# Kernel optimization log

Hardware: AMD Instinct MI355X
Metric: run time of the kernel (lower is better)

## Reference

```python
import jax, jax.numpy as jnp
import numpy as np

N_NODES = 50000
N_EDGES = 1600000
N_GRAPHS = 512
VOCAB = 1000
EMB = 32
HID = 64
N_CLASS = 2


def setup_inputs() -> dict:
    key = jax.random.key(0)
    ks = jax.random.split(key, 12)
    x_ids = jax.random.randint(ks[0], (N_NODES,), 0, VOCAB)
    edge_index = jax.random.randint(ks[1], (2, N_EDGES), 0, N_NODES)
    batch = jnp.sort(jax.random.randint(ks[2], (N_NODES,), 0, N_GRAPHS))
    def s(k, shape, fan):
        return jax.random.normal(k, shape, jnp.float32) * (1.0 / np.sqrt(fan))
    return {
        "x_ids": x_ids,
        "edge_index": edge_index,
        "batch": batch,
        "embed": s(ks[3], (VOCAB, EMB), EMB),
        "w1_l": s(ks[4], (EMB, HID), EMB),
        "b1": jnp.zeros((HID,), jnp.float32),
        "w1_r": s(ks[5], (EMB, HID), EMB),
        "w2_l": s(ks[6], (HID, HID), HID),
        "b2": jnp.zeros((HID,), jnp.float32),
        "w2_r": s(ks[7], (HID, HID), HID),
        "w_out": s(ks[8], (HID, N_CLASS), HID),
        "b_out": jnp.zeros((N_CLASS,), jnp.float32),
    }


def _sage(x, src, dst, w_l, b, w_r):
    # PyG SAGEConv (aggr='mean'): out = lin_l(mean_{j in N(i)} x_j) + lin_r(x_i)
    msg_sum = jax.ops.segment_sum(x[src], dst, num_segments=N_NODES)  # [N, d]
    deg = jax.ops.segment_sum(jnp.ones((src.shape[0],), x.dtype), dst,
                              num_segments=N_NODES)
    mean = msg_sum / jnp.maximum(deg, 1.0)[:, None]
    return mean @ w_l + b + x @ w_r


def reference(x_ids, edge_index, batch, embed, w1_l, b1, w1_r,
              w2_l, b2, w2_r, w_out, b_out):
    src, dst = edge_index[0], edge_index[1]
    x = embed[x_ids]                                  # [N, emb]
    x = jax.nn.relu(_sage(x, src, dst, w1_l, b1, w1_r))  # [N, hid]
    x = jax.nn.relu(_sage(x, src, dst, w2_l, b2, w2_r))  # [N, hid]
    # global_mean_pool over batch segments
    gsum = jax.ops.segment_sum(x, batch, num_segments=N_GRAPHS)
    gcnt = jax.ops.segment_sum(jnp.ones((N_NODES,), x.dtype), batch,
                               num_segments=N_GRAPHS)
    pooled = gsum / jnp.maximum(gcnt, 1.0)[:, None]   # [G, hid]
    return pooled @ w_out + b_out                     # [G, n_class]
```

## Files before the change

kernel.cpp:

```cpp
#include <hip/hip_runtime.h>
#include <hip/hip_bf16.h>

#define N_NODES 50000
#define N_EDGES 1600000
#define N_GRAPHS 512
#define VOCAB 1000
#define EMB 32
#define HID 64
#define N_CLASS 2

#define MAXDEG 96

#define NVEC (N_EDGES / 4)
#define SORT_VPB 1024
#define SORT_BLOCKS ((NVEC + SORT_VPB - 1) / SORT_VPB)
#define BSHIFT 8
#define BUCKET_NODES 256
#define NBUCK ((N_NODES + BUCKET_NODES - 1) / BUCKET_NODES)

#define L2P_BLOCKS 768
#define L2P_WAVES (L2P_BLOCKS * 4)
#define L2P_CHUNK ((N_NODES + L2P_WAVES - 1) / L2P_WAVES)

typedef int iv4 __attribute__((ext_vector_type(4)));
typedef unsigned long long u64;

__device__ __forceinline__ float rdlane(float v, int k) {
    return __int_as_float(__builtin_amdgcn_readlane(__float_as_int(v), k));
}

__global__ __launch_bounds__(256) void hist_kernel(const int* __restrict__ dst,
                                                   int* __restrict__ hist) {
    __shared__ int lh[NBUCK];
    for (int b = threadIdx.x; b < NBUCK; b += 256) lh[b] = 0;
    __syncthreads();
    const iv4* dst4 = (const iv4*)dst;
    int vbase = blockIdx.x * SORT_VPB;
    #pragma unroll
    for (int t = 0; t < 4; ++t) {
        int v = vbase + t * 256 + threadIdx.x;
        if (v < NVEC) {
            iv4 d4 = __builtin_nontemporal_load(&dst4[v]);
            atomicAdd(&lh[d4.x >> BSHIFT], 1);
            atomicAdd(&lh[d4.y >> BSHIFT], 1);
            atomicAdd(&lh[d4.z >> BSHIFT], 1);
            atomicAdd(&lh[d4.w >> BSHIFT], 1);
        }
    }
    __syncthreads();
    for (int b = threadIdx.x; b < NBUCK; b += 256)
        hist[b * SORT_BLOCKS + blockIdx.x] = lh[b];
}

__global__ __launch_bounds__(256) void scan_rows_kernel(int* __restrict__ hist,
                                                        int* __restrict__ btot) {
    int* row = hist + (size_t)blockIdx.x * SORT_BLOCKS;
    __shared__ int wsum[4];
    int tid = threadIdx.x, lane = tid & 63, w = tid >> 6;
    int carry = 0;
    for (int base = 0; base < SORT_BLOCKS; base += 256) {
        int idx = base + tid;
        int v = (idx < SORT_BLOCKS) ? row[idx] : 0;
        int inc = v;
        #pragma unroll
        for (int off = 1; off < 64; off <<= 1) {
            int n = __shfl_up(inc, off, 64);
            if (lane >= off) inc += n;
        }
        if (lane == 63) wsum[w] = inc;
        __syncthreads();
        int woff = 0;
        #pragma unroll
        for (int k = 0; k < 4; ++k) if (k < w) woff += wsum[k];
        if (idx < SORT_BLOCKS) row[idx] = carry + woff + inc - v;
        carry += wsum[0] + wsum[1] + wsum[2] + wsum[3];
        __syncthreads();
    }
    if (tid == 0) btot[blockIdx.x] = carry;
}

__global__ __launch_bounds__(256) void scan_btot_kernel(const int* __restrict__ btot,
                                                        int* __restrict__ boff) {
    __shared__ int wsum[4];
    int tid = threadIdx.x, lane = tid & 63, w = tid >> 6;
    int v = (tid < NBUCK) ? btot[tid] : 0;
    int inc = v;
    #pragma unroll
    for (int off = 1; off < 64; off <<= 1) {
        int n = __shfl_up(inc, off, 64);
        if (lane >= off) inc += n;
    }
    if (lane == 63) wsum[w] = inc;
    __syncthreads();
    int woff = 0;
    #pragma unroll
    for (int k = 0; k < 4; ++k) if (k < w) woff += wsum[k];
    if (tid < NBUCK) boff[tid] = woff + inc - v;
    if (tid == 0) boff[NBUCK] = wsum[0] + wsum[1] + wsum[2] + wsum[3];
}

__global__ __launch_bounds__(256) void scatter_kernel(const int* __restrict__ src,
        const int* __restrict__ dst, const int* __restrict__ x_ids,
        const int* __restrict__ hist, const int* __restrict__ boff,
        u64* __restrict__ ebuf) {
    __shared__ int lbase[NBUCK];
    for (int b = threadIdx.x; b < NBUCK; b += 256)
        lbase[b] = hist[b * SORT_BLOCKS + blockIdx.x] + boff[b];
    __syncthreads();
    const iv4* dst4 = (const iv4*)dst;
    const iv4* src4 = (const iv4*)src;
    int vbase = blockIdx.x * SORT_VPB;
    #pragma unroll
    for (int t = 0; t < 4; ++t) {
        int v = vbase + t * 256 + threadIdx.x;
        if (v < NVEC) {
            iv4 d4 = __builtin_nontemporal_load(&dst4[v]);
            iv4 s4 = __builtin_nontemporal_load(&src4[v]);
            int pay0 = (x_ids[s4.x] << 16) | s4.x;
            int pay1 = (x_ids[s4.y] << 16) | s4.y;
            int pay2 = (x_ids[s4.z] << 16) | s4.z;
            int pay3 = (x_ids[s4.w] << 16) | s4.w;
            int p0 = atomicAdd(&lbase[d4.x >> BSHIFT], 1);
            int p1 = atomicAdd(&lbase[d4.y >> BSHIFT], 1);
            int p2 = atomicAdd(&lbase[d4.z >> BSHIFT], 1);
            int p3 = atomicAdd(&lbase[d4.w >> BSHIFT], 1);
            ebuf[p0] = ((u64)(unsigned)d4.x << 32) | (unsigned)pay0;
            ebuf[p1] = ((u64)(unsigned)d4.y << 32) | (unsigned)pay1;
            ebuf[p2] = ((u64)(unsigned)d4.z << 32) | (unsigned)pay2;
            ebuf[p3] = ((u64)(unsigned)d4.w << 32) | (unsigned)pay3;
        }
    }
}

__global__ __launch_bounds__(256) void csr_bucket_kernel(const u64* __restrict__ ebuf,
        const int* __restrict__ boff, int* __restrict__ cursor, int* __restrict__ csr) {
    int b = blockIdx.x;
    __shared__ int cur[BUCKET_NODES];
    for (int r = threadIdx.x; r < BUCKET_NODES; r += 256) cur[r] = 0;
    __syncthreads();
    int base = boff[b];
    int end  = boff[b + 1];
    int node0 = b << BSHIFT;
    for (int i = base + threadIdx.x; i < end; i += 256) {
        u64 e = ebuf[i];
        int d = (int)(e >> 32);
        int pay = (int)(e & 0xffffffffu);
        int pos = atomicAdd(&cur[d - node0], 1);
        csr[d * MAXDEG + pos] = pay;
    }
    __syncthreads();
    for (int r = threadIdx.x; r < BUCKET_NODES; r += 256) {
        int d = node0 + r;
        if (d < N_NODES) cursor[d] = cur[r];
    }
}

__global__ void precompute_e1_kernel(const float* __restrict__ embed,
                                     const float* __restrict__ w1l,
                                     const float* __restrict__ w1r,
                                     __hip_bfloat16* __restrict__ e1b,
                                     float* __restrict__ e1r) {
    int id = blockIdx.x * blockDim.x + threadIdx.x;
    if (id >= VOCAB * HID) return;
    int v = id >> 6, j = id & 63;
    float a = 0.0f, b = 0.0f;
    #pragma unroll
    for (int k = 0; k < EMB; ++k) {
        float ev = embed[v * EMB + k];
        a = fmaf(ev, w1l[k * HID + j], a);
        b = fmaf(ev, w1r[k * HID + j], b);
    }
    e1b[id] = __float2bfloat16(a);
    e1r[id] = b;
}

__global__ __launch_bounds__(256) void agg1_lin1_kernel(
        const int* __restrict__ x_ids, const int* __restrict__ csr,
        const int* __restrict__ deg_arr, const __hip_bfloat16* __restrict__ e1b,
        const float* __restrict__ e1r, const float* __restrict__ b1,
        float* __restrict__ h1, __hip_bfloat16* __restrict__ h1b) {
    int id = blockIdx.x * blockDim.x + threadIdx.x;
    int i = __builtin_amdgcn_readfirstlane(id >> 6);
    int j = threadIdx.x & 63;
    int s = i * MAXDEG;
    int deg = deg_arr[i];
    int e = s + deg;
    float s0 = 0.f, s1 = 0.f, s2 = 0.f, s3 = 0.f;
    float s4 = 0.f, s5 = 0.f, s6 = 0.f, s7 = 0.f;
    int k = s;
    for (; k + 8 <= e; k += 8) {
        int c0 = csr[k]     >> 16, c1 = csr[k + 1] >> 16;
        int c2 = csr[k + 2] >> 16, c3 = csr[k + 3] >> 16;
        int c4 = csr[k + 4] >> 16, c5 = csr[k + 5] >> 16;
        int c6 = csr[k + 6] >> 16, c7 = csr[k + 7] >> 16;
        s0 += (float)e1b[c0 * HID + j];
        s1 += (float)e1b[c1 * HID + j];
        s2 += (float)e1b[c2 * HID + j];
        s3 += (float)e1b[c3 * HID + j];
        s4 += (float)e1b[c4 * HID + j];
        s5 += (float)e1b[c5 * HID + j];
        s6 += (float)e1b[c6 * HID + j];
        s7 += (float)e1b[c7 * HID + j];
    }
    for (; k < e; ++k) s0 += (float)e1b[(csr[k] >> 16) * HID + j];
    float mean = ((s0 + s1) + (s2 + s3) + (s4 + s5) + (s6 + s7)) / fmaxf((float)deg, 1.0f);
    float h = fmaxf(mean + b1[j] + e1r[x_ids[i] * HID + j], 0.0f);
    int o = i * HID + j;
    h1[o] = h;
    h1b[o] = __float2bfloat16(h);
}

__global__ __launch_bounds__(256) void agg2_mean_kernel(
        const __hip_bfloat16* __restrict__ h1b, const int* __restrict__ csr,
        const int* __restrict__ deg_arr, float* __restrict__ mean2) {
    int id = blockIdx.x * blockDim.x + threadIdx.x;
    int i = __builtin_amdgcn_readfirstlane(id >> 6);
    int j = threadIdx.x & 63;
    int s = i * MAXDEG;
    int deg = deg_arr[i];
    int e = s + deg;
    float s0 = 0.f, s1 = 0.f, s2 = 0.f, s3 = 0.f;
    float s4 = 0.f, s5 = 0.f, s6 = 0.f, s7 = 0.f;
    int k = s;
    for (; k + 8 <= e; k += 8) {
        int n0 = csr[k]     & 0xFFFF, n1 = csr[k + 1] & 0xFFFF;
        int n2 = csr[k + 2] & 0xFFFF, n3 = csr[k + 3] & 0xFFFF;
        int n4 = csr[k + 4] & 0xFFFF, n5 = csr[k + 5] & 0xFFFF;
        int n6 = csr[k + 6] & 0xFFFF, n7 = csr[k + 7] & 0xFFFF;
        s0 += (float)h1b[n0 * HID + j];
        s1 += (float)h1b[n1 * HID + j];
        s2 += (float)h1b[n2 * HID + j];
        s3 += (float)h1b[n3 * HID + j];
        s4 += (float)h1b[n4 * HID + j];
        s5 += (float)h1b[n5 * HID + j];
        s6 += (float)h1b[n6 * HID + j];
        s7 += (float)h1b[n7 * HID + j];
    }
    for (; k < e; ++k) s0 += (float)h1b[(csr[k] & 0xFFFF) * HID + j];
    float mean = ((s0 + s1) + (s2 + s3) + (s4 + s5) + (s6 + s7)) / fmaxf((float)deg, 1.0f);
    mean2[i * HID + j] = mean;
}

__global__ __launch_bounds__(256) void lin2_pool_kernel(
        const float* __restrict__ mean2, const float* __restrict__ h1,
        const float* __restrict__ w2l, const float* __restrict__ b2,
        const float* __restrict__ w2r, const int* __restrict__ batch,
        float* __restrict__ gsum) {
    int lane = threadIdx.x & 63;
    int wv = (blockIdx.x * blockDim.x + threadIdx.x) >> 6;
    int i0 = wv * L2P_CHUNK;
    int i1 = i0 + L2P_CHUNK; if (i1 > N_NODES) i1 = N_NODES;
    if (i0 >= N_NODES) return;
    float wl[HID], wr[HID];
    #pragma unroll
    for (int k = 0; k < HID; ++k) {
        wl[k] = w2l[k * HID + lane];
        wr[k] = w2r[k * HID + lane];
    }
    float bj = b2[lane];
    int curg = __builtin_amdgcn_readfirstlane(batch[i0]);
    float accp = 0.0f;
    float m = mean2[i0 * HID + lane];
    float h = h1[i0 * HID + lane];
    for (int i = i0; i < i1; ++i) {
        float mn = 0.f, hn = 0.f;
        if (i + 1 < i1) {
            mn = mean2[(i + 1) * HID + lane];
            hn = h1[(i + 1) * HID + lane];
        }
        int g = __builtin_amdgcn_readfirstlane(batch[i]);
        if (g != curg) {
            atomicAdd(&gsum[curg * HID + lane], accp);
            accp = 0.0f;
            curg = g;
        }
        float z = bj;
        #pragma unroll
        for (int k = 0; k < HID; ++k)
            z = fmaf(rdlane(m, k), wl[k], fmaf(rdlane(h, k), wr[k], z));
        accp += fmaxf(z, 0.0f);
        m = mn; h = hn;
    }
    atomicAdd(&gsum[curg * HID + lane], accp);
}

__global__ void out_kernel(const float* __restrict__ gsum, const int* __restrict__ batch,
                           const float* __restrict__ w_out, const float* __restrict__ b_out,
                           float* __restrict__ out) {
    int id = blockIdx.x * blockDim.x + threadIdx.x;
    if (id >= N_GRAPHS * N_CLASS) return;
    int g = id >> 1, c = id & 1;
    int lo = 0, hi = N_NODES;
    while (lo < hi) { int mid = (lo + hi) >> 1; if (batch[mid] < g) lo = mid + 1; else hi = mid; }
    int first = lo;
    lo = 0; hi = N_NODES;
    while (lo < hi) { int mid = (lo + hi) >> 1; if (batch[mid] <= g) lo = mid + 1; else hi = mid; }
    float cnt = (float)(lo - first);
    float inv = 1.0f / fmaxf(cnt, 1.0f);
    float acc = b_out[c];
    #pragma unroll
    for (int j = 0; j < HID; ++j)
        acc = fmaf(gsum[g * HID + j] * inv, w_out[j * N_CLASS + c], acc);
    out[id] = acc;
}


extern "C" void kernel_launch(void* const* d_in, const int* in_sizes, int n_in,
                              void* d_out, int out_size, void* d_ws, size_t ws_size,
                              hipStream_t stream) {
    const int*   x_ids = (const int*)d_in[0];
    const int*   edge  = (const int*)d_in[1];
    const int*   batch = (const int*)d_in[2];
    const float* embed = (const float*)d_in[3];
    const float* w1l   = (const float*)d_in[4];
    const float* b1    = (const float*)d_in[5];
    const float* w1r   = (const float*)d_in[6];
    const float* w2l   = (const float*)d_in[7];
    const float* b2    = (const float*)d_in[8];
    const float* w2r   = (const float*)d_in[9];
    const float* wout  = (const float*)d_in[10];
    const float* bout  = (const float*)d_in[11];
    const int* src = edge;
    const int* dst = edge + N_EDGES;
    float* out = (float*)d_out;

    char* ws = (char*)d_ws;
    size_t off = 0;
    auto alloc = [&](size_t bytes) -> void* {
        void* p = ws + off;
        off += (bytes + 255) & ~(size_t)255;
        return p;
    };
    float*           h1     = (float*)alloc((size_t)N_NODES * HID * 4);
    __hip_bfloat16*  h1b    = (__hip_bfloat16*)alloc((size_t)N_NODES * HID * 2);
    float*           mean2  = (float*)alloc((size_t)N_NODES * HID * 4);
    int*             csr    = (int*)alloc((size_t)N_NODES * MAXDEG * 4);
    int*             cursor = (int*)alloc((size_t)N_NODES * 4);
    int*             hist   = (int*)alloc((size_t)NBUCK * SORT_BLOCKS * 4);
    int*             btot   = (int*)alloc((size_t)NBUCK * 4);
    int*             boff   = (int*)alloc((size_t)(NBUCK + 1) * 4);
    __hip_bfloat16*  e1b    = (__hip_bfloat16*)alloc((size_t)VOCAB * HID * 2);
    float*           e1r    = (float*)alloc((size_t)VOCAB * HID * 4);
    float*           gsum   = (float*)alloc((size_t)N_GRAPHS * HID * 4);

    u64* ebuf = (u64*)mean2;

    hipMemsetAsync(gsum, 0, (size_t)N_GRAPHS * HID * 4, stream);

    const int B = 256;
    precompute_e1_kernel<<<(VOCAB * HID + B - 1) / B, B, 0, stream>>>(embed, w1l, w1r, e1b, e1r);

    hist_kernel<<<SORT_BLOCKS, B, 0, stream>>>(dst, hist);
    scan_rows_kernel<<<NBUCK, B, 0, stream>>>(hist, btot);
    scan_btot_kernel<<<1, B, 0, stream>>>(btot, boff);
    scatter_kernel<<<SORT_BLOCKS, B, 0, stream>>>(src, dst, x_ids, hist, boff, ebuf);
    csr_bucket_kernel<<<NBUCK, B, 0, stream>>>(ebuf, boff, cursor, csr);

    agg1_lin1_kernel<<<N_NODES * HID / B, B, 0, stream>>>(x_ids, csr, cursor,
                                                          e1b, e1r, b1, h1, h1b);
    agg2_mean_kernel<<<N_NODES * HID / B, B, 0, stream>>>(h1b, csr, cursor, mean2);
    lin2_pool_kernel<<<L2P_BLOCKS, B, 0, stream>>>(mean2, h1, w2l, b2, w2r, batch, gsum);
    out_kernel<<<(N_GRAPHS * N_CLASS + B - 1) / B, B, 0, stream>>>(gsum, batch, wout, bout, out);
}
```

Measured before the change: 232.5 us.

## Process eight nodes per wave with 16-byte vectorized bf16 row gathers in aggregation

Both neighbor-aggregation kernels are remapped so that each wave handles 8 nodes instead of one. Each lane owns 8 contiguous features and loads them with a single 16-byte load, replacing one 2-byte load per lane per neighbor. CSR indices are read four at a time, and outputs are written as vector stores. This is meant to cut the memory instruction count and the per-neighbor scalar overhead of the gathers. In exchange, lanes within a wave now follow different node degrees, which adds divergence, and the iv4 CSR read can go past the node's degree into padding slots.

```diff
diff --git a/kernel.cpp b/kernel.cpp
--- a/kernel.cpp
+++ b/kernel.cpp
@@ -18,13 +18,29 @@
 #define BUCKET_NODES 256
 #define NBUCK ((N_NODES + BUCKET_NODES - 1) / BUCKET_NODES)
 
+#define AGG_THREADS (N_NODES * 8)
+#define AGG_BLOCKS ((AGG_THREADS + 255) / 256)
+
 #define L2P_BLOCKS 768
 #define L2P_WAVES (L2P_BLOCKS * 4)
 #define L2P_CHUNK ((N_NODES + L2P_WAVES - 1) / L2P_WAVES)
 
 typedef int iv4 __attribute__((ext_vector_type(4)));
+typedef unsigned short us;
+typedef us usv8 __attribute__((ext_vector_type(8)));
+typedef float fv4 __attribute__((ext_vector_type(4)));
 typedef unsigned long long u64;
 
+__device__ __forceinline__ float bf2f(us u) {
+    union { unsigned int i; float f; } c;
+    c.i = ((unsigned int)u) << 16;
+    return c.f;
+}
+__device__ __forceinline__ us f2bf(float f) {
+    union { __hip_bfloat16 b; us u; } c;
+    c.b = __float2bfloat16(f);
+    return c.u;
+}
 __device__ __forceinline__ float rdlane(float v, int k) {
     return __int_as_float(__builtin_amdgcn_readlane(__float_as_int(v), k));
 }
@@ -158,7 +174,7 @@
 __global__ void precompute_e1_kernel(const float* __restrict__ embed,
                                      const float* __restrict__ w1l,
                                      const float* __restrict__ w1r,
-                                     __hip_bfloat16* __restrict__ e1b,
+                                     us* __restrict__ e1b,
                                      float* __restrict__ e1r) {
     int id = blockIdx.x * blockDim.x + threadIdx.x;
     if (id >= VOCAB * HID) return;
@@ -170,75 +186,93 @@
         a = fmaf(ev, w1l[k * HID + j], a);
         b = fmaf(ev, w1r[k * HID + j], b);
     }
-    e1b[id] = __float2bfloat16(a);
+    e1b[id] = f2bf(a);
     e1r[id] = b;
 }
 
 __global__ __launch_bounds__(256) void agg1_lin1_kernel(
         const int* __restrict__ x_ids, const int* __restrict__ csr,
-        const int* __restrict__ deg_arr, const __hip_bfloat16* __restrict__ e1b,
+        const int* __restrict__ deg_arr, const us* __restrict__ e1b,
         const float* __restrict__ e1r, const float* __restrict__ b1,
-        float* __restrict__ h1, __hip_bfloat16* __restrict__ h1b) {
-    int id = blockIdx.x * blockDim.x + threadIdx.x;
-    int i = __builtin_amdgcn_readfirstlane(id >> 6);
-    int j = threadIdx.x & 63;
-    int s = i * MAXDEG;
-    int deg = deg_arr[i];
-    int e = s + deg;
-    float s0 = 0.f, s1 = 0.f, s2 = 0.f, s3 = 0.f;
-    float s4 = 0.f, s5 = 0.f, s6 = 0.f, s7 = 0.f;
-    int k = s;
-    for (; k + 8 <= e; k += 8) {
-        int c0 = csr[k]     >> 16, c1 = csr[k + 1] >> 16;
-        int c2 = csr[k + 2] >> 16, c3 = csr[k + 3] >> 16;
-        int c4 = csr[k + 4] >> 16, c5 = csr[k + 5] >> 16;
-        int c6 = csr[k + 6] >> 16, c7 = csr[k + 7] >> 16;
-        s0 += (float)e1b[c0 * HID + j];
-        s1 += (float)e1b[c1 * HID + j];
-        s2 += (float)e1b[c2 * HID + j];
-        s3 += (float)e1b[c3 * HID + j];
-        s4 += (float)e1b[c4 * HID + j];
-        s5 += (float)e1b[c5 * HID + j];
-        s6 += (float)e1b[c6 * HID + j];
-        s7 += (float)e1b[c7 * HID + j];
-    }
-    for (; k < e; ++k) s0 += (float)e1b[(csr[k] >> 16) * HID + j];
-    float mean = ((s0 + s1) + (s2 + s3) + (s4 + s5) + (s6 + s7)) / fmaxf((float)deg, 1.0f);
-    float h = fmaxf(mean + b1[j] + e1r[x_ids[i] * HID + j], 0.0f);
-    int o = i * HID + j;
-    h1[o] = h;
-    h1b[o] = __float2bfloat16(h);
+        float* __restrict__ h1, us* __restrict__ h1b) {
+    int tid = blockIdx.x * blockDim.x + threadIdx.x;
+    int lane = threadIdx.x & 63;
+    int g = lane >> 3, c8 = lane & 7;
+    int node = (tid >> 6) * 8 + g;
+    bool valid = node < N_NODES;
+    int nclamp = valid ? node : 0;
+    int deg = valid ? deg_arr[nclamp] : 0;
+    const int* crow = csr + (size_t)nclamp * MAXDEG;
+    float a0=0.f,a1=0.f,a2=0.f,a3=0.f,a4=0.f,a5=0.f,a6=0.f,a7=0.f;
+    for (int k = 0; k < deg; k += 4) {
+        iv4 cv = *(const iv4*)(crow + k);
+        #define GATH1(CVAL, T)                                                   \
+        if (k + (T) < deg) {                                                     \
+            int cls = (CVAL) >> 16;                                              \
+            usv8 r = *(const usv8*)(e1b + cls * HID + c8 * 8);                   \
+            a0 += bf2f(r[0]); a1 += bf2f(r[1]); a2 += bf2f(r[2]); a3 += bf2f(r[3]); \
+            a4 += bf2f(r[4]); a5 += bf2f(r[5]); a6 += bf2f(r[6]); a7 += bf2f(r[7]); \
+        }
+        GATH1(cv.x, 0) GATH1(cv.y, 1) GATH1(cv.z, 2) GATH1(cv.w, 3)
+        #undef GATH1
+    }
+    if (!valid) return;
+    float inv = 1.0f / fmaxf((float)deg, 1.0f);
+    int xid = x_ids[nclamp];
+    const fv4* er = (const fv4*)(e1r + xid * HID + c8 * 8);
+    fv4 e0 = er[0], e1v = er[1];
+    const fv4* bb = (const fv4*)(b1 + c8 * 8);
+    fv4 b0 = bb[0], b1v = bb[1];
+    fv4 h0, h1v;
+    h0.x = fmaxf(a0 * inv + b0.x + e0.x, 0.0f);
+    h0.y = fmaxf(a1 * inv + b0.y + e0.y, 0.0f);
+    h0.z = fmaxf(a2 * inv + b0.z + e0.z, 0.0f);
+    h0.w = fmaxf(a3 * inv + b0.w + e0.w, 0.0f);
+    h1v.x = fmaxf(a4 * inv + b1v.x + e1v.x, 0.0f);
+    h1v.y = fmaxf(a5 * inv + b1v.y + e1v.y, 0.0f);
+    h1v.z = fmaxf(a6 * inv + b1v.z + e1v.z, 0.0f);
+    h1v.w = fmaxf(a7 * inv + b1v.w + e1v.w, 0.0f);
+    int o = node * HID + c8 * 8;
+    *(fv4*)(h1 + o) = h0;
+    *(fv4*)(h1 + o + 4) = h1v;
+    usv8 hb;
+    hb[0] = f2bf(h0.x); hb[1] = f2bf(h0.y); hb[2] = f2bf(h0.z); hb[3] = f2bf(h0.w);
+    hb[4] = f2bf(h1v.x); hb[5] = f2bf(h1v.y); hb[6] = f2bf(h1v.z); hb[7] = f2bf(h1v.w);
+    *(usv8*)(h1b + o) = hb;
 }
 
 __global__ __launch_bounds__(256) void agg2_mean_kernel(
-        const __hip_bfloat16* __restrict__ h1b, const int* __restrict__ csr,
+        const us* __restrict__ h1b, const int* __restrict__ csr,
         const int* __restrict__ deg_arr, float* __restrict__ mean2) {
-    int id = blockIdx.x * blockDim.x + threadIdx.x;
-    int i = __builtin_amdgcn_readfirstlane(id >> 6);
-    int j = threadIdx.x & 63;
-    int s = i * MAXDEG;
-    int deg = deg_arr[i];
-    int e = s + deg;
-    float s0 = 0.f, s1 = 0.f, s2 = 0.f, s3 = 0.f;
-    float s4 = 0.f, s5 = 0.f, s6 = 0.f, s7 = 0.f;
-    int k = s;
-    for (; k + 8 <= e; k += 8) {
-        int n0 = csr[k]     & 0xFFFF, n1 = csr[k + 1] & 0xFFFF;
-        int n2 = csr[k + 2] & 0xFFFF, n3 = csr[k + 3] & 0xFFFF;
-        int n4 = csr[k + 4] & 0xFFFF, n5 = csr[k + 5] & 0xFFFF;
-        int n6 = csr[k + 6] & 0xFFFF, n7 = csr[k + 7] & 0xFFFF;
-        s0 += (float)h1b[n0 * HID + j];
-        s1 += (float)h1b[n1 * HID + j];
-        s2 += (float)h1b[n2 * HID + j];
-        s3 += (float)h1b[n3 * HID + j];
-        s4 += (float)h1b[n4 * HID + j];
-        s5 += (float)h1b[n5 * HID + j];
-        s6 += (float)h1b[n6 * HID + j];
-        s7 += (float)h1b[n7 * HID + j];
-    }
-    for (; k < e; ++k) s0 += (float)h1b[(csr[k] & 0xFFFF) * HID + j];
-    float mean = ((s0 + s1) + (s2 + s3) + (s4 + s5) + (s6 + s7)) / fmaxf((float)deg, 1.0f);
-    mean2[i * HID + j] = mean;
+    int tid = blockIdx.x * blockDim.x + threadIdx.x;
+    int lane = threadIdx.x & 63;
+    int g = lane >> 3, c8 = lane & 7;
+    int node = (tid >> 6) * 8 + g;
+    bool valid = node < N_NODES;
+    int nclamp = valid ? node : 0;
+    int deg = valid ? deg_arr[nclamp] : 0;
+    const int* crow = csr + (size_t)nclamp * MAXDEG;
+    float a0=0.f,a1=0.f,a2=0.f,a3=0.f,a4=0.f,a5=0.f,a6=0.f,a7=0.f;
+    for (int k = 0; k < deg; k += 4) {
+        iv4 cv = *(const iv4*)(crow + k);
+        #define GATH2(CVAL, T)                                                   \
+        if (k + (T) < deg) {                                                     \
+            int nb = (CVAL) & 0xFFFF;                                            \
+            usv8 r = *(const usv8*)(h1b + nb * HID + c8 * 8);                    \
+            a0 += bf2f(r[0]); a1 += bf2f(r[1]); a2 += bf2f(r[2]); a3 += bf2f(r[3]); \
+            a4 += bf2f(r[4]); a5 += bf2f(r[5]); a6 += bf2f(r[6]); a7 += bf2f(r[7]); \
+        }
+        GATH2(cv.x, 0) GATH2(cv.y, 1) GATH2(cv.z, 2) GATH2(cv.w, 3)
+        #undef GATH2
+    }
+    if (!valid) return;
+    float inv = 1.0f / fmaxf((float)deg, 1.0f);
+    fv4 m0, m1;
+    m0.x = a0 * inv; m0.y = a1 * inv; m0.z = a2 * inv; m0.w = a3 * inv;
+    m1.x = a4 * inv; m1.y = a5 * inv; m1.z = a6 * inv; m1.w = a7 * inv;
+    int o = node * HID + c8 * 8;
+    *(fv4*)(mean2 + o) = m0;
+    *(fv4*)(mean2 + o + 4) = m1;
 }
 
 __global__ __launch_bounds__(256) void lin2_pool_kernel(
@@ -331,17 +365,17 @@
         off += (bytes + 255) & ~(size_t)255;
         return p;
     };
-    float*           h1     = (float*)alloc((size_t)N_NODES * HID * 4);
-    __hip_bfloat16*  h1b    = (__hip_bfloat16*)alloc((size_t)N_NODES * HID * 2);
-    float*           mean2  = (float*)alloc((size_t)N_NODES * HID * 4);
-    int*             csr    = (int*)alloc((size_t)N_NODES * MAXDEG * 4);
-    int*             cursor = (int*)alloc((size_t)N_NODES * 4);
-    int*             hist   = (int*)alloc((size_t)NBUCK * SORT_BLOCKS * 4);
-    int*             btot   = (int*)alloc((size_t)NBUCK * 4);
-    int*             boff   = (int*)alloc((size_t)(NBUCK + 1) * 4);
-    __hip_bfloat16*  e1b    = (__hip_bfloat16*)alloc((size_t)VOCAB * HID * 2);
-    float*           e1r    = (float*)alloc((size_t)VOCAB * HID * 4);
-    float*           gsum   = (float*)alloc((size_t)N_GRAPHS * HID * 4);
+    float*  h1     = (float*)alloc((size_t)N_NODES * HID * 4);
+    us*     h1b    = (us*)alloc((size_t)N_NODES * HID * 2);
+    float*  mean2  = (float*)alloc((size_t)N_NODES * HID * 4);
+    int*    csr    = (int*)alloc((size_t)N_NODES * MAXDEG * 4);
+    int*    cursor = (int*)alloc((size_t)N_NODES * 4);
+    int*    hist   = (int*)alloc((size_t)NBUCK * SORT_BLOCKS * 4);
+    int*    btot   = (int*)alloc((size_t)NBUCK * 4);
+    int*    boff   = (int*)alloc((size_t)(NBUCK + 1) * 4);
+    us*     e1b    = (us*)alloc((size_t)VOCAB * HID * 2);
+    float*  e1r    = (float*)alloc((size_t)VOCAB * HID * 4);
+    float*  gsum   = (float*)alloc((size_t)N_GRAPHS * HID * 4);
 
     u64* ebuf = (u64*)mean2;
 
@@ -356,9 +390,9 @@
     scatter_kernel<<<SORT_BLOCKS, B, 0, stream>>>(src, dst, x_ids, hist, boff, ebuf);
     csr_bucket_kernel<<<NBUCK, B, 0, stream>>>(ebuf, boff, cursor, csr);
 
-    agg1_lin1_kernel<<<N_NODES * HID / B, B, 0, stream>>>(x_ids, csr, cursor,
-                                                          e1b, e1r, b1, h1, h1b);
-    agg2_mean_kernel<<<N_NODES * HID / B, B, 0, stream>>>(h1b, csr, cursor, mean2);
+    agg1_lin1_kernel<<<AGG_BLOCKS, B, 0, stream>>>(x_ids, csr, cursor,
+                                                   e1b, e1r, b1, h1, h1b);
+    agg2_mean_kernel<<<AGG_BLOCKS, B, 0, stream>>>(h1b, csr, cursor, mean2);
     lin2_pool_kernel<<<L2P_BLOCKS, B, 0, stream>>>(mean2, h1, w2l, b2, w2r, batch, gsum);
     out_kernel<<<(N_GRAPHS * N_CLASS + B - 1) / B, B, 0, stream>>>(gsum, batch, wout, bout, out);
 }
```

Measured after the change: 223.2 us. 1.04x faster.
